# Kernel optimization log

Hardware: AMD Instinct MI355X
Metric: run time of the kernel (lower is better)

## Reference

```python
import jax, jax.numpy as jnp
import numpy as np

D_MODEL = 1024
NUM_HEADS = 16
HEAD_DIM = D_MODEL // NUM_HEADS  # 64
MAX_REL = 512
NUM_EMB = 2 * MAX_REL + 1  # 1025
B, L = 2, 2048


def _glorot(key, shape):
    fan_in, fan_out = shape[0], shape[1]
    lim = jnp.sqrt(6.0 / (fan_in + fan_out))
    return jax.random.uniform(key, shape, jnp.float32, -lim, lim)


def setup_inputs() -> dict:
    key = jax.random.key(0)
    ks = jax.random.split(key, 9)
    return {
        "query": jax.random.normal(ks[0], (B, L, D_MODEL), jnp.float32),
        "key": jax.random.normal(ks[1], (B, L, D_MODEL), jnp.float32),
        "value": jax.random.normal(ks[2], (B, L, D_MODEL), jnp.float32),
        "wq": _glorot(ks[3], (D_MODEL, D_MODEL)), "bq": jnp.zeros((D_MODEL,), jnp.float32),
        "wk": _glorot(ks[4], (D_MODEL, D_MODEL)), "bk": jnp.zeros((D_MODEL,), jnp.float32),
        "wv": _glorot(ks[5], (D_MODEL, D_MODEL)), "bv": jnp.zeros((D_MODEL,), jnp.float32),
        "wo": _glorot(ks[6], (D_MODEL, D_MODEL)), "bo": jnp.zeros((D_MODEL,), jnp.float32),
        "rel_emb": _glorot(ks[7], (NUM_EMB, HEAD_DIM)),
    }


def _split_heads(x):
    b, l, _ = x.shape
    return x.reshape(b, l, NUM_HEADS, HEAD_DIM).transpose(0, 2, 1, 3)  # (b,h,l,d)


def reference(query, key, value, wq, bq, wk, bk, wv, bv, wo, bo, rel_emb):
    q = _split_heads(query @ wq + bq)  # (b,h,l,d)
    k = _split_heads(key @ wk + bk)
    v = _split_heads(value @ wv + bv)

    # content scores: (b,h,l,l)
    content = jnp.einsum('bhid,bhjd->bhij', q, k)

    # relative position scores. Original gathers E[clip(j-i)] -> (L,L,d) then
    # einsum('bhid,ijd->bhij'). Equivalent & cheaper: project q onto all
    # relative embeddings once, then gather along the relative-index axis.
    idx = jnp.arange(q.shape[2])
    final_mat = jnp.clip(idx[None, :] - idx[:, None], -MAX_REL, MAX_REL) + MAX_REL  # (L,L)
    q_rel = jnp.einsum('bhid,rd->bhir', q, rel_emb)  # (b,h,l,num_emb)
    position = jnp.take_along_axis(q_rel, final_mat[None, None, :, :], axis=-1)  # (b,h,l,l)

    scores = (content + position) / jnp.sqrt(jnp.float32(HEAD_DIM))
    weights = jax.nn.softmax(scores, axis=-1)  # no mask, dropout off (inference)
    out = jnp.einsum('bhij,bhjd->bhid', weights, v)  # (b,h,l,d)

    out = out.transpose(0, 2, 1, 3).reshape(query.shape[0], -1, D_MODEL)
    return out @ wo + bo
```

## Files before the change

kernel.cpp:

```cpp
#include <hip/hip_runtime.h>
#include <hip/hip_bf16.h>


typedef __attribute__((ext_vector_type(8))) short short8;
typedef __attribute__((ext_vector_type(4))) float floatx4;

#define L_SEQ 2048
#define D_MODEL 1024
#define NHEAD 16
#define DH 64
#define BH 32
#define MROWS 4096

__device__ inline float b2f(short s) {
    unsigned int u = ((unsigned int)(unsigned short)s) << 16;
    float f; __builtin_memcpy(&f, &u, 4); return f;
}
__device__ inline short f2b(float f) {
    unsigned int u; __builtin_memcpy(&u, &f, 4);
    u += 0x7fffu + ((u >> 16) & 1u);
    return (short)(u >> 16);
}
__device__ inline unsigned int pack2(float a, float b) {
    __hip_bfloat162 h = __float22bfloat162_rn(make_float2(a, b));
    unsigned int u; __builtin_memcpy(&u, &h, 4); return u;
}
__device__ inline void st2(short* p, unsigned int v) {
    __builtin_memcpy(p, &v, 4);
}
__device__ inline void async_cp16(short* lds, const short* g) {
    __builtin_amdgcn_global_load_lds(
        (const __attribute__((address_space(1))) unsigned int*)g,
        (__attribute__((address_space(3))) unsigned int*)lds, 16, 0, 0);
}

__global__ __launch_bounds__(256) void detect_dtype(
        const unsigned short* __restrict__ q, int* __restrict__ flag) {
    __shared__ int s[256];
    int tid = threadIdx.x, cnt = 0;
    for (int i = tid; i < 65536; i += 256)
        if ((q[i] & 0x7F80u) == 0x7F80u) cnt++;
    s[tid] = cnt; __syncthreads();
    for (int st = 128; st; st >>= 1) {
        if (tid < st) s[tid] += s[tid + st];
        __syncthreads();
    }
    if (tid == 0) *flag = (s[0] > 4) ? 1 : 0;
}

__global__ __launch_bounds__(256) void norm_small(
        const void* __restrict__ bq, const void* __restrict__ bk,
        const void* __restrict__ bv, const void* __restrict__ bo,
        const void* __restrict__ rel, float* __restrict__ bias4,
        short* __restrict__ relb, const int* __restrict__ flagp) {
    const int f32 = *flagp;
    int t = blockIdx.x * 256 + threadIdx.x;
    if (t < 4096) {
        const void* src = (t < 1024) ? bq : (t < 2048) ? bk : (t < 3072) ? bv : bo;
        int i = t & 1023;
        bias4[t] = f32 ? ((const float*)src)[i] : b2f(((const short*)src)[i]);
    } else if (t < 4096 + 65600) {
        int i = t - 4096;
        relb[i] = f32 ? f2b(((const float*)rel)[i]) : ((const short*)rel)[i];
    }
}

__global__ __launch_bounds__(256) void transpose4(
        const void* __restrict__ w0, const void* __restrict__ w1,
        const void* __restrict__ w2, const void* __restrict__ w3,
        short* __restrict__ dst, const int* __restrict__ flagp) {
    const int f32 = *flagp;
    __shared__ short tile[32][33];
    const void* src = (blockIdx.z == 0) ? w0 : (blockIdx.z == 1) ? w1
                    : (blockIdx.z == 2) ? w2 : w3;
    short* d = dst + (size_t)blockIdx.z * (D_MODEL * D_MODEL);
    int x = blockIdx.x * 32 + threadIdx.x;
    int y0 = blockIdx.y * 32;
    for (int yy = threadIdx.y; yy < 32; yy += 8) {
        size_t idx = (size_t)(y0 + yy) * D_MODEL + x;
        tile[yy][threadIdx.x] = f32 ? f2b(((const float*)src)[idx])
                                    : ((const short*)src)[idx];
    }
    __syncthreads();
    int x0 = blockIdx.x * 32;
    for (int yy = threadIdx.y; yy < 32; yy += 8)
        d[(size_t)(x0 + yy) * D_MODEL + y0 + threadIdx.x] = tile[threadIdx.x][yy];
}

__global__ __launch_bounds__(256) void convert3(
        const float* __restrict__ q, const float* __restrict__ k,
        const float* __restrict__ v, short* __restrict__ abf_q,
        short* __restrict__ abf_k, short* __restrict__ abf_v,
        const int* __restrict__ flagp) {
    if (!*flagp) return;
    const int z = blockIdx.y;
    const float* src = (z == 0) ? q : (z == 1) ? k : v;
    short* dst = (z == 0) ? abf_q : (z == 1) ? abf_k : abf_v;
    size_t i8 = ((size_t)blockIdx.x * 256 + threadIdx.x) * 8;
    float4 f0 = *(const float4*)(&src[i8]);
    float4 f1 = *(const float4*)(&src[i8 + 4]);
    uint4 s;
    s.x = pack2(f0.x, f0.y); s.y = pack2(f0.z, f0.w);
    s.z = pack2(f1.x, f1.y); s.w = pack2(f1.z, f1.w);
    *(uint4*)(&dst[i8]) = s;
}

__global__ __launch_bounds__(256) void proj_gemm(
        const void* __restrict__ Aq, const void* __restrict__ Ak,
        const void* __restrict__ Av, const short* __restrict__ Cq,
        const short* __restrict__ Ck, const short* __restrict__ Cv,
        const short* __restrict__ WT, const float* __restrict__ bias4,
        short* __restrict__ Qout, const int* __restrict__ flagp) {
    const int f32 = *flagp;
    const int z = blockIdx.z;
    const short* A_ = f32 ? ((z == 0) ? Cq : (z == 1) ? Ck : Cv)
                          : (const short*)((z == 0) ? Aq : (z == 1) ? Ak : Av);
    const short* BT = WT + (size_t)z * (D_MODEL * D_MODEL);
    const float* bias = bias4 + z * 1024;
    short* C = Qout + (size_t)z * ((size_t)MROWS * D_MODEL);
    const int K = D_MODEL;

    __shared__ short Alds[128 * 32];
    __shared__ short Blds[128 * 32];
    const int tid = threadIdx.x;
    const int w = tid >> 6, lane = tid & 63, cl = lane & 15, quad = lane >> 4;
    const int wr = w >> 1, wc = w & 1;
    int wg = blockIdx.x + 8 * blockIdx.y;
    wg = (wg & 7) * 32 + (wg >> 3);
    const int m0 = (wg >> 3) * 128, n0 = (wg & 7) * 128;
    const int grow = lane >> 2, gcol = (lane & 3) * 8;

    floatx4 acc[4][4];
    for (int i = 0; i < 4; i++)
        for (int j = 0; j < 4; j++)
            acc[i][j] = {0.f, 0.f, 0.f, 0.f};

    for (int k0 = 0; k0 < K; k0 += 32) {
        for (int s = 0; s < 2; s++) {
            int r = w * 32 + s * 16;
            async_cp16(&Blds[r * 32], &BT[(size_t)(n0 + r + grow) * K + k0 + gcol]);
            async_cp16(&Alds[r * 32], &A_[(size_t)(m0 + r + grow) * K + k0 + gcol]);
        }
        __syncthreads();

        short8 af[4], bfr[4];
        for (int mt = 0; mt < 4; mt++)
            af[mt] = *(const short8*)(&Alds[(wr * 64 + mt * 16 + cl) * 32 + quad * 8]);
        for (int nt = 0; nt < 4; nt++)
            bfr[nt] = *(const short8*)(&Blds[(wc * 64 + nt * 16 + cl) * 32 + quad * 8]);
        for (int mt = 0; mt < 4; mt++)
            for (int nt = 0; nt < 4; nt++)
                acc[mt][nt] = __builtin_amdgcn_mfma_f32_16x16x32_bf16(
                    af[mt], bfr[nt], acc[mt][nt], 0, 0, 0);
        __syncthreads();
    }

    for (int nt = 0; nt < 4; nt++) {
        int n = n0 + wc * 64 + nt * 16 + cl;
        float bv = bias[n];
        int h = n >> 6, d = n & 63;
        for (int mt = 0; mt < 4; mt++) {
            for (int r = 0; r < 4; r++) {
                int m = m0 + wr * 64 + mt * 16 + quad * 4 + r;
                float v = acc[mt][nt][r] + bv;
                int b = m >> 11, i = m & 2047;
                if (z < 2)
                    C[(((size_t)(b * NHEAD + h)) * L_SEQ + i) * DH + d] = f2b(v);
                else
                    C[(((size_t)(b * NHEAD + h)) * DH + d) * L_SEQ + i] = f2b(v);
            }
        }
    }
}

__global__ __launch_bounds__(256) void out_gemm(
        const short* __restrict__ A, const short* __restrict__ BT,
        const float* __restrict__ bias, void* __restrict__ C_,
        const int* __restrict__ flagp) {
    const int f32 = *flagp;
    const int K = D_MODEL, N = D_MODEL;
    __shared__ short Alds[128 * 32];
    __shared__ short Blds[64 * 32];
    const int tid = threadIdx.x;
    const int w = tid >> 6, lane = tid & 63, cl = lane & 15, quad = lane >> 4;
    const int wr = w >> 1, wc = w & 1;
    int wg = blockIdx.x + 16 * blockIdx.y;
    wg = (wg & 7) * 64 + (wg >> 3);
    const int m0 = (wg >> 4) * 128, n0 = (wg & 15) * 64;
    const int grow = lane >> 2, gcol = (lane & 3) * 8;

    floatx4 acc[4][2];
    for (int i = 0; i < 4; i++)
        for (int j = 0; j < 2; j++)
            acc[i][j] = {0.f, 0.f, 0.f, 0.f};

    for (int k0 = 0; k0 < K; k0 += 32) {
        for (int s = 0; s < 2; s++) {
            int r = w * 32 + s * 16;
            async_cp16(&Alds[r * 32], &A[(size_t)(m0 + r + grow) * K + k0 + gcol]);
        }
        {
            int r = w * 16;
            async_cp16(&Blds[r * 32], &BT[(size_t)(n0 + r + grow) * K + k0 + gcol]);
        }
        __syncthreads();

        short8 af[4], bfr[2];
        for (int mt = 0; mt < 4; mt++)
            af[mt] = *(const short8*)(&Alds[(wr * 64 + mt * 16 + cl) * 32 + quad * 8]);
        for (int nt = 0; nt < 2; nt++)
            bfr[nt] = *(const short8*)(&Blds[(wc * 32 + nt * 16 + cl) * 32 + quad * 8]);
        for (int mt = 0; mt < 4; mt++)
            for (int nt = 0; nt < 2; nt++)
                acc[mt][nt] = __builtin_amdgcn_mfma_f32_16x16x32_bf16(
                    af[mt], bfr[nt], acc[mt][nt], 0, 0, 0);
        __syncthreads();
    }

    for (int nt = 0; nt < 2; nt++) {
        int n = n0 + wc * 32 + nt * 16 + cl;
        float bv = bias[n];
        for (int mt = 0; mt < 4; mt++) {
            for (int r = 0; r < 4; r++) {
                int m = m0 + wr * 64 + mt * 16 + quad * 4 + r;
                float v = acc[mt][nt][r] + bv;
                if (f32) ((float*)C_)[(size_t)m * N + n] = v;
                else     ((short*)C_)[(size_t)m * N + n] = f2b(v);
            }
        }
    }
}

__global__ __launch_bounds__(256) void attn_kernel(
        const short* __restrict__ Q, const short* __restrict__ K,
        const short* __restrict__ VT, const short* __restrict__ rel,
        short* __restrict__ out) {
    const int tid = threadIdx.x;
    const int w = tid >> 6, lane = tid & 63, cl = lane & 15, quad = lane >> 4;
    int wg = blockIdx.x + 32 * blockIdx.y;
    wg = (wg & 7) * 128 + (wg >> 3);
    const int bh = wg >> 5, b = bh >> 4, h = bh & 15;
    const int I0 = (wg & 31) * 64;
    const int iw0 = I0 + w * 16;

    const short* Qp = Q + (size_t)bh * L_SEQ * DH;
    const short* Kp = K + (size_t)bh * L_SEQ * DH;
    const short* Vp = VT + (size_t)bh * DH * L_SEQ;

    __shared__ short Klds[64 * 64];
    __shared__ short Vtlds[64 * 64];
    __shared__ short PpLds[4][16 * 86];
    __shared__ short Plds[4][16 * 64];

    short* PpW = &PpLds[w][0];
    short* PW  = &Plds[w][0];

    short8 aq[2];
    for (int c = 0; c < 2; c++)
        aq[c] = *(const short8*)(&Qp[(size_t)(iw0 + cl) * DH + c * 32 + quad * 8]);

    const float SCALE2 = 0.125f * 1.44269504088896340736f;
    const float FMAX = 32.0f;

    float addlo, addhi;
    {
        floatx4 Dc = {0.f, 0.f, 0.f, 0.f};
        int eidx = (cl == 1) ? 1024 : 0;
        for (int c = 0; c < 2; c++) {
            short8 ae = *(const short8*)(&rel[(size_t)eidx * DH + c * 32 + quad * 8]);
            Dc = __builtin_amdgcn_mfma_f32_16x16x32_bf16(ae, aq[c], Dc, 0, 0, 0);
        }
        float pcl = __shfl(Dc[0], cl, 64);
        float pch = __shfl(Dc[1], cl, 64);
        addlo = fmaf(pcl, SCALE2, -FMAX);
        addhi = fmaf(pch, SCALE2, -FMAX);
    }

    floatx4 O[4];
    for (int dt = 0; dt < 4; dt++) O[dt] = {0.f, 0.f, 0.f, 0.f};
    float lsum = 0.f;

    const int srow = tid >> 2;
    const int spair = (tid & 3) * 2;

    for (int j0 = 0; j0 < L_SEQ; j0 += 64) {
        for (int s = 0; s < 2; s++) {
            int chunk = spair + s;
            int pos = chunk ^ (srow & 7);
            *(short8*)(&Klds[srow * 64 + pos * 8]) =
                *(const short8*)(&Kp[(size_t)(j0 + srow) * DH + chunk * 8]);
            *(short8*)(&Vtlds[srow * 64 + pos * 8]) =
                *(const short8*)(&Vp[(size_t)srow * L_SEQ + j0 + chunk * 8]);
        }
        __syncthreads();

        const bool hi_clamp = (j0 - iw0 - 15) >= 512;
        const bool lo_clamp = (j0 + 63 - iw0) <= -512;
        const bool banded = !(hi_clamp || lo_clamp);
        const float addc = hi_clamp ? addhi : addlo;

        floatx4 St[4];
        for (int jt = 0; jt < 4; jt++) {
            St[jt] = {0.f, 0.f, 0.f, 0.f};
            int row = jt * 16 + cl;
            for (int c = 0; c < 2; c++) {
                int pos = ((4 * c + quad) ^ (cl & 7)) * 8;
                short8 bk = *(const short8*)(&Klds[row * 64 + pos]);
                St[jt] = __builtin_amdgcn_mfma_f32_16x16x32_bf16(bk, aq[c], St[jt], 0, 0, 0);
            }
        }

        if (banded) {
            floatx4 Pt[5];
            for (int pt = 0; pt < 5; pt++) Pt[pt] = {0.f, 0.f, 0.f, 0.f};
            const int base = j0 - iw0 - 15;
            for (int pt = 0; pt < 5; pt++) {
                int raw = pt * 16 + cl + base;
                int idx = (raw < -512 ? -512 : (raw > 512 ? 512 : raw)) + 512;
                const short* ep = rel + (size_t)idx * DH;
                for (int c = 0; c < 2; c++) {
                    short8 be = *(const short8*)(&ep[c * 32 + quad * 8]);
                    Pt[pt] = __builtin_amdgcn_mfma_f32_16x16x32_bf16(be, aq[c], Pt[pt], 0, 0, 0);
                }
            }
            for (int pt = 0; pt < 5; pt++) {
                int t = pt * 16 + quad * 4;
                st2(&PpW[cl * 86 + t],     pack2(Pt[pt][0], Pt[pt][1]));
                st2(&PpW[cl * 86 + t + 2], pack2(Pt[pt][2], Pt[pt][3]));
            }
            for (int jt = 0; jt < 4; jt++)
                for (int r = 0; r < 4; r++) {
                    int t = jt * 16 + quad * 4 + r - cl + 15;
                    float pos = b2f(PpW[cl * 86 + t]);
                    St[jt][r] = fmaf(St[jt][r], SCALE2, fmaf(pos, SCALE2, -FMAX));
                }
        } else {
            for (int jt = 0; jt < 4; jt++)
                for (int r = 0; r < 4; r++)
                    St[jt][r] = fmaf(St[jt][r], SCALE2, addc);
        }

        for (int jt = 0; jt < 4; jt++)
            for (int r = 0; r < 4; r++) {
                float p = __builtin_amdgcn_exp2f(St[jt][r]);
                St[jt][r] = p;
                lsum += p;
            }

        for (int jt = 0; jt < 4; jt++)
            for (int pr = 0; pr < 2; pr++) {
                int jl = jt * 16 + quad * 4 + pr * 2;
                int addr = cl * 64 + ((jl >> 3) ^ (cl & 7)) * 8 + (jl & 7);
                st2(&PW[addr], pack2(St[jt][2 * pr], St[jt][2 * pr + 1]));
            }

        for (int c = 0; c < 2; c++) {
            int ppos = ((4 * c + quad) ^ (cl & 7)) * 8;
            short8 bp = *(const short8*)(&PW[cl * 64 + ppos]);
            for (int dt = 0; dt < 4; dt++) {
                int row = dt * 16 + cl;
                int vpos = ((4 * c + quad) ^ (cl & 7)) * 8;
                short8 av = *(const short8*)(&Vtlds[row * 64 + vpos]);
                O[dt] = __builtin_amdgcn_mfma_f32_16x16x32_bf16(av, bp, O[dt], 0, 0, 0);
            }
        }
        __syncthreads();
    }

    lsum += __shfl_xor(lsum, 16, 64);
    lsum += __shfl_xor(lsum, 32, 64);
    float inv = 1.0f / lsum;

    for (int dt = 0; dt < 4; dt++)
        for (int pr = 0; pr < 2; pr++) {
            int jl = dt * 16 + quad * 4 + pr * 2;
            int addr = cl * 64 + ((jl >> 3) ^ (cl & 7)) * 8 + (jl & 7);
            st2(&PW[addr], pack2(O[dt][2 * pr] * inv, O[dt][2 * pr + 1] * inv));
        }
    size_t obase = ((size_t)b * L_SEQ + iw0 + cl) * D_MODEL + h * DH;
    for (int s = 0; s < 2; s++) {
        int c2 = quad * 2 + s;
        short8 o = *(const short8*)(&PW[cl * 64 + (c2 ^ (cl & 7)) * 8]);
        *(short8*)(&out[obase + c2 * 8]) = o;
    }
}

extern "C" void kernel_launch(void* const* d_in, const int* in_sizes, int n_in,
                              void* d_out, int out_size, void* d_ws, size_t ws_size,
                              hipStream_t stream) {
    const void* query = d_in[0];
    const void* key   = d_in[1];
    const void* value = d_in[2];
    const void* wq = d_in[3];  const void* bq = d_in[4];
    const void* wk = d_in[5];  const void* bk = d_in[6];
    const void* wv = d_in[7];  const void* bv = d_in[8];
    const void* wo = d_in[9];  const void* bo = d_in[10];
    const void* rel = d_in[11];

    int* flag = (int*)d_ws;
    short* ws = (short*)d_ws + 16;
    const size_t WSZ = (size_t)D_MODEL * D_MODEL;
    const size_t TSZ = (size_t)MROWS * D_MODEL;
    short* WT   = ws;
    short* Qw   = ws + 4 * WSZ;
    short* Kw   = Qw + TSZ;
    short* Vtw  = Kw + TSZ;
    short* Attw = Vtw + TSZ;
    float* bias4 = (float*)(Attw + TSZ);
    short* relb  = (short*)(bias4 + 4096);

    short* Cq = (short*)d_out;
    short* Ck = (short*)d_out + TSZ;
    short* Cv = Attw;

    {
        long qb = (long)in_sizes[0];
        const long FP32B = (long)MROWS * D_MODEL * 4;
        const long BF16B = (long)MROWS * D_MODEL * 2;
        int fhost = (qb == FP32B) ? 1 : (qb == BF16B) ? 0 : -1;
        if (fhost >= 0)
            hipMemsetAsync(flag, fhost, 4, stream);
        else
            detect_dtype<<<1, 256, 0, stream>>>((const unsigned short*)query, flag);
    }

    norm_small<<<273, 256, 0, stream>>>(bq, bk, bv, bo, rel, bias4, relb, flag);
    transpose4<<<dim3(32, 32, 4), dim3(32, 8), 0, stream>>>(wq, wk, wv, wo, WT, flag);

    convert3<<<dim3(2048, 3), 256, 0, stream>>>(
        (const float*)query, (const float*)key, (const float*)value,
        Cq, Ck, Cv, flag);

    proj_gemm<<<dim3(8, 32, 3), 256, 0, stream>>>(query, key, value,
                                                  Cq, Ck, Cv, WT, bias4,
                                                  Qw, flag);

    attn_kernel<<<dim3(L_SEQ / 64, BH), 256, 0, stream>>>(Qw, Kw, Vtw, relb, Attw);

    out_gemm<<<dim3(16, 32), 256, 0, stream>>>(Attw, WT + 3 * WSZ, bias4 + 3072,
                                               d_out, flag);
}
```

Before: 377.1 us.

## Merge prep kernels into one launch and store fp32 rel-pos band in LDS

Merges the three preprocessing kernels (weight transpose, input conversion, bias and relative-embedding normalisation) into a single launch, so two kernel launches and their gaps go away. In the attention kernel, the banded relative-position tile is now kept in LDS as fp32 and written with wide 16-byte stores rather than packed to bf16. The softmax probabilities and the output are written with 8-byte stores, reusing one unified per-wave LDS buffer. In exchange the attention kernel uses more LDS, which may lower occupancy, and the merged prep kernel branches on block id.

Result: no change. 375.0 us (-0.5%).

```diff
diff --git a/kernel.cpp b/kernel.cpp
--- a/kernel.cpp
+++ b/kernel.cpp
@@ -11,6 +11,7 @@
 #define DH 64
 #define BH 32
 #define MROWS 4096
+#define PPAD 92
 
 __device__ inline float b2f(short s) {
     unsigned int u = ((unsigned int)(unsigned short)s) << 16;
@@ -27,6 +28,15 @@
 }
 __device__ inline void st2(short* p, unsigned int v) {
     __builtin_memcpy(p, &v, 4);
+}
+__device__ inline void st4(short* p, unsigned int a, unsigned int b) {
+    unsigned int v[2] = {a, b}; __builtin_memcpy(p, v, 8);
+}
+__device__ inline void stf4(short* p, floatx4 v) {
+    __builtin_memcpy(p, &v, 16);
+}
+__device__ inline float ldf(const short* p) {
+    float f; __builtin_memcpy(&f, p, 4); return f;
 }
 __device__ inline void async_cp16(short* lds, const short* g) {
     __builtin_amdgcn_global_load_lds(
@@ -48,61 +58,66 @@
     if (tid == 0) *flag = (s[0] > 4) ? 1 : 0;
 }
 
-__global__ __launch_bounds__(256) void norm_small(
+__global__ __launch_bounds__(256) void prep_all(
+        const void* __restrict__ w0, const void* __restrict__ w1,
+        const void* __restrict__ w2, const void* __restrict__ w3,
         const void* __restrict__ bq, const void* __restrict__ bk,
         const void* __restrict__ bv, const void* __restrict__ bo,
-        const void* __restrict__ rel, float* __restrict__ bias4,
-        short* __restrict__ relb, const int* __restrict__ flagp) {
+        const void* __restrict__ rel,
+        const float* __restrict__ q, const float* __restrict__ k,
+        const float* __restrict__ v,
+        short* __restrict__ WT, float* __restrict__ bias4,
+        short* __restrict__ relb,
+        short* __restrict__ Cq, short* __restrict__ Ck, short* __restrict__ Cv,
+        const int* __restrict__ flagp) {
     const int f32 = *flagp;
-    int t = blockIdx.x * 256 + threadIdx.x;
-    if (t < 4096) {
-        const void* src = (t < 1024) ? bq : (t < 2048) ? bk : (t < 3072) ? bv : bo;
-        int i = t & 1023;
-        bias4[t] = f32 ? ((const float*)src)[i] : b2f(((const short*)src)[i]);
-    } else if (t < 4096 + 65600) {
-        int i = t - 4096;
-        relb[i] = f32 ? f2b(((const float*)rel)[i]) : ((const short*)rel)[i];
-    }
-}
-
-__global__ __launch_bounds__(256) void transpose4(
-        const void* __restrict__ w0, const void* __restrict__ w1,
-        const void* __restrict__ w2, const void* __restrict__ w3,
-        short* __restrict__ dst, const int* __restrict__ flagp) {
-    const int f32 = *flagp;
-    __shared__ short tile[32][33];
-    const void* src = (blockIdx.z == 0) ? w0 : (blockIdx.z == 1) ? w1
-                    : (blockIdx.z == 2) ? w2 : w3;
-    short* d = dst + (size_t)blockIdx.z * (D_MODEL * D_MODEL);
-    int x = blockIdx.x * 32 + threadIdx.x;
-    int y0 = blockIdx.y * 32;
-    for (int yy = threadIdx.y; yy < 32; yy += 8) {
-        size_t idx = (size_t)(y0 + yy) * D_MODEL + x;
-        tile[yy][threadIdx.x] = f32 ? f2b(((const float*)src)[idx])
-                                    : ((const short*)src)[idx];
-    }
-    __syncthreads();
-    int x0 = blockIdx.x * 32;
-    for (int yy = threadIdx.y; yy < 32; yy += 8)
-        d[(size_t)(x0 + yy) * D_MODEL + y0 + threadIdx.x] = tile[threadIdx.x][yy];
-}
-
-__global__ __launch_bounds__(256) void convert3(
-        const float* __restrict__ q, const float* __restrict__ k,
-        const float* __restrict__ v, short* __restrict__ abf_q,
-        short* __restrict__ abf_k, short* __restrict__ abf_v,
-        const int* __restrict__ flagp) {
-    if (!*flagp) return;
-    const int z = blockIdx.y;
-    const float* src = (z == 0) ? q : (z == 1) ? k : v;
-    short* dst = (z == 0) ? abf_q : (z == 1) ? abf_k : abf_v;
-    size_t i8 = ((size_t)blockIdx.x * 256 + threadIdx.x) * 8;
-    float4 f0 = *(const float4*)(&src[i8]);
-    float4 f1 = *(const float4*)(&src[i8 + 4]);
-    uint4 s;
-    s.x = pack2(f0.x, f0.y); s.y = pack2(f0.z, f0.w);
-    s.z = pack2(f1.x, f1.y); s.w = pack2(f1.z, f1.w);
-    *(uint4*)(&dst[i8]) = s;
+    const int id = blockIdx.x;
+    const int tid = threadIdx.x;
+
+    if (id < 4096) {
+        __shared__ short tile[32][33];
+        const int wz = id >> 10, rem = id & 1023;
+        const int bx = rem & 31, by = rem >> 5;
+        const int tx = tid & 31, ty = tid >> 5;
+        const void* src = (wz == 0) ? w0 : (wz == 1) ? w1 : (wz == 2) ? w2 : w3;
+        short* d = WT + (size_t)wz * (D_MODEL * D_MODEL);
+        int x = bx * 32 + tx;
+        int y0 = by * 32;
+        for (int yy = ty; yy < 32; yy += 8) {
+            size_t idx = (size_t)(y0 + yy) * D_MODEL + x;
+            tile[yy][tx] = f32 ? f2b(((const float*)src)[idx])
+                               : ((const short*)src)[idx];
+        }
+        __syncthreads();
+        int x0 = bx * 32;
+        for (int yy = ty; yy < 32; yy += 8)
+            d[(size_t)(x0 + yy) * D_MODEL + y0 + tx] = tile[tx][yy];
+    } else if (id < 10240) {
+        if (!f32) return;
+        const int cid = id - 4096;
+        const int z = cid >> 11;
+        const int bx = cid & 2047;
+        const float* src = (z == 0) ? q : (z == 1) ? k : v;
+        short* dst = (z == 0) ? Cq : (z == 1) ? Ck : Cv;
+        size_t i8 = ((size_t)bx * 256 + tid) * 8;
+        float4 f0 = *(const float4*)(&src[i8]);
+        float4 f1 = *(const float4*)(&src[i8 + 4]);
+        uint4 s;
+        s.x = pack2(f0.x, f0.y); s.y = pack2(f0.z, f0.w);
+        s.z = pack2(f1.x, f1.y); s.w = pack2(f1.z, f1.w);
+        *(uint4*)(&dst[i8]) = s;
+    } else {
+        int t = (id - 10240) * 256 + tid;
+        if (t < 4096) {
+            const void* src = (t < 1024) ? bq : (t < 2048) ? bk
+                            : (t < 3072) ? bv : bo;
+            int i = t & 1023;
+            bias4[t] = f32 ? ((const float*)src)[i] : b2f(((const short*)src)[i]);
+        } else if (t < 4096 + 65600) {
+            int i = t - 4096;
+            relb[i] = f32 ? f2b(((const float*)rel)[i]) : ((const short*)rel)[i];
+        }
+    }
 }
 
 __global__ __launch_bounds__(256) void proj_gemm(
@@ -249,11 +264,9 @@
 
     __shared__ short Klds[64 * 64];
     __shared__ short Vtlds[64 * 64];
-    __shared__ short PpLds[4][16 * 86];
-    __shared__ short Plds[4][16 * 64];
-
-    short* PpW = &PpLds[w][0];
-    short* PW  = &Plds[w][0];
+    __shared__ short Ulds[4][16 * PPAD * 2];
+
+    short* UW = &Ulds[w][0];
 
     short8 aq[2];
     for (int c = 0; c < 2; c++)
@@ -325,13 +338,12 @@
             }
             for (int pt = 0; pt < 5; pt++) {
                 int t = pt * 16 + quad * 4;
-                st2(&PpW[cl * 86 + t],     pack2(Pt[pt][0], Pt[pt][1]));
-                st2(&PpW[cl * 86 + t + 2], pack2(Pt[pt][2], Pt[pt][3]));
+                stf4(&UW[(cl * PPAD + t) * 2], Pt[pt]);
             }
             for (int jt = 0; jt < 4; jt++)
                 for (int r = 0; r < 4; r++) {
                     int t = jt * 16 + quad * 4 + r - cl + 15;
-                    float pos = b2f(PpW[cl * 86 + t]);
+                    float pos = ldf(&UW[(cl * PPAD + t) * 2]);
                     St[jt][r] = fmaf(St[jt][r], SCALE2, fmaf(pos, SCALE2, -FMAX));
                 }
         } else {
@@ -347,16 +359,16 @@
                 lsum += p;
             }
 
-        for (int jt = 0; jt < 4; jt++)
-            for (int pr = 0; pr < 2; pr++) {
-                int jl = jt * 16 + quad * 4 + pr * 2;
-                int addr = cl * 64 + ((jl >> 3) ^ (cl & 7)) * 8 + (jl & 7);
-                st2(&PW[addr], pack2(St[jt][2 * pr], St[jt][2 * pr + 1]));
-            }
+        for (int jt = 0; jt < 4; jt++) {
+            int jl = jt * 16 + quad * 4;
+            int addr = cl * 64 + ((jl >> 3) ^ (cl & 7)) * 8 + (jl & 7);
+            st4(&UW[addr], pack2(St[jt][0], St[jt][1]),
+                           pack2(St[jt][2], St[jt][3]));
+        }
 
         for (int c = 0; c < 2; c++) {
             int ppos = ((4 * c + quad) ^ (cl & 7)) * 8;
-            short8 bp = *(const short8*)(&PW[cl * 64 + ppos]);
+            short8 bp = *(const short8*)(&UW[cl * 64 + ppos]);
             for (int dt = 0; dt < 4; dt++) {
                 int row = dt * 16 + cl;
                 int vpos = ((4 * c + quad) ^ (cl & 7)) * 8;
@@ -371,16 +383,16 @@
     lsum += __shfl_xor(lsum, 32, 64);
     float inv = 1.0f / lsum;
 
-    for (int dt = 0; dt < 4; dt++)
-        for (int pr = 0; pr < 2; pr++) {
-            int jl = dt * 16 + quad * 4 + pr * 2;
-            int addr = cl * 64 + ((jl >> 3) ^ (cl & 7)) * 8 + (jl & 7);
-            st2(&PW[addr], pack2(O[dt][2 * pr] * inv, O[dt][2 * pr + 1] * inv));
-        }
+    for (int dt = 0; dt < 4; dt++) {
+        int jl = dt * 16 + quad * 4;
+        int addr = cl * 64 + ((jl >> 3) ^ (cl & 7)) * 8 + (jl & 7);
+        st4(&UW[addr], pack2(O[dt][0] * inv, O[dt][1] * inv),
+                       pack2(O[dt][2] * inv, O[dt][3] * inv));
+    }
     size_t obase = ((size_t)b * L_SEQ + iw0 + cl) * D_MODEL + h * DH;
     for (int s = 0; s < 2; s++) {
         int c2 = quad * 2 + s;
-        short8 o = *(const short8*)(&PW[cl * 64 + (c2 ^ (cl & 7)) * 8]);
+        short8 o = *(const short8*)(&UW[cl * 64 + (c2 ^ (cl & 7)) * 8]);
         *(short8*)(&out[obase + c2 * 8]) = o;
     }
 }
@@ -424,12 +436,10 @@
             detect_dtype<<<1, 256, 0, stream>>>((const unsigned short*)query, flag);
     }
 
-    norm_small<<<273, 256, 0, stream>>>(bq, bk, bv, bo, rel, bias4, relb, flag);
-    transpose4<<<dim3(32, 32, 4), dim3(32, 8), 0, stream>>>(wq, wk, wv, wo, WT, flag);
-
-    convert3<<<dim3(2048, 3), 256, 0, stream>>>(
+    prep_all<<<10513, 256, 0, stream>>>(
+        wq, wk, wv, wo, bq, bk, bv, bo, rel,
         (const float*)query, (const float*)key, (const float*)value,
-        Cq, Ck, Cv, flag);
+        WT, bias4, relb, Cq, Ck, Cv, flag);
 
     proj_gemm<<<dim3(8, 32, 3), 256, 0, stream>>>(query, key, value,
                                                   Cq, Ck, Cv, WT, bias4,
```
